# Optimization experiments

Measured on AMD Instinct MI355X. Metric: run time of the kernel, lower is better.

Reference implementation:

```python
import jax, jax.numpy as jnp
import numpy as np

DECAY = 0.8
COMMITMENT_WEIGHT = 1.0
EPS = 1e-5


def setup_inputs() -> dict:
    key = jax.random.key(0)
    k1, k2, k3 = jax.random.split(key, 3)
    B, T, D, K = 16, 2048, 512, 8192
    x = jax.random.normal(k1, (B, T, D), dtype=jnp.float32)
    embed = jax.random.normal(k2, (D, K), dtype=jnp.float32)
    cluster_size = jnp.ones((K,), dtype=jnp.float32)
    embed_avg = jax.random.normal(k3, (D, K), dtype=jnp.float32)
    return {"x": x, "embed": embed, "cluster_size": cluster_size, "embed_avg": embed_avg}


def reference(x, embed, cluster_size, embed_avg):
    B, T, D = x.shape
    K = embed.shape[1]
    flat = x.reshape(-1, D)  # [N, D]

    # squared L2 distance to each code: ||f||^2 - 2 f.e + ||e||^2  -> [N, K]
    dist = (flat * flat).sum(-1, keepdims=True) \
        - 2.0 * (flat @ embed) \
        + (embed * embed).sum(0, keepdims=True)
    embed_ind = jnp.argmin(dist, axis=1)  # [N] (== argmax of -dist)

    quantize = jnp.take(embed.T, embed_ind, axis=0).reshape(B, T, D)

    # ---- EMA codebook statistics (training-mode buffer updates) ----
    onehot_sum = jnp.zeros((K,), dtype=flat.dtype).at[embed_ind].add(1.0)  # [K]
    # flat.T @ onehot == segment-sum of tokens per code, transposed -> [D, K]
    embed_sum = jax.ops.segment_sum(flat, embed_ind, num_segments=K).T
    new_cluster_size = cluster_size * DECAY + (1.0 - DECAY) * onehot_sum
    new_embed_avg = embed_avg * DECAY + (1.0 - DECAY) * embed_sum
    n = new_cluster_size.sum()
    cs = (new_cluster_size + EPS) / (n + K * EPS) * n
    new_embed = new_embed_avg / cs[None, :]
    # (random re-init of unused codes is omitted: non-deterministic side effect)

    commitment_loss = jnp.mean((jax.lax.stop_gradient(quantize) - x) ** 2) * COMMITMENT_WEIGHT
    quantize_st = x + jax.lax.stop_gradient(quantize - x)  # straight-through

    return (quantize_st, embed_ind.reshape(B, T), commitment_loss,
            new_embed, new_cluster_size, new_embed_avg)
```

## Files before the change

### kernel.cpp

```cpp
#include <hip/hip_runtime.h>

#define NTOK   32768
#define DDIM   512
#define KCODES 8192
#define DK     (DDIM * KCODES)
#define DECAYF 0.8f
#define EPSF   1e-5f

using short8 = __attribute__((ext_vector_type(8))) short;
using f32x4  = __attribute__((ext_vector_type(4))) float;

#define WS_ESUMT   0
#define WS_ONEHOT  DK
#define WS_ENORM   (DK + 8192)
#define WS_SCAL    (DK + 16384)
#define WS_PART    (DK + 16400)
#define WS_EMBEDT  (WS_PART + 2 * NTOK)
#define WS_EHI     (WS_EMBEDT + DK)
#define WS_ELO     (WS_EHI + DK / 2)
#define WS_ZERO_BYTES ((size_t)(DK + 16400) * 4)

__device__ __forceinline__ unsigned short bf16rne(float f) {
  unsigned u = __float_as_uint(f);
  unsigned r = u + 0x7FFFu + ((u >> 16) & 1u);
  return (unsigned short)(r >> 16);
}

__device__ __forceinline__ void gload_lds16(const unsigned short* g, unsigned short* l) {
  __builtin_amdgcn_global_load_lds(
      (const __attribute__((address_space(1))) unsigned int*)g,
      (__attribute__((address_space(3))) unsigned int*)l, 16, 0, 0);
}

__global__ __launch_bounds__(256) void split_x_kernel(
    const float* __restrict__ x, unsigned short* __restrict__ hi,
    unsigned short* __restrict__ lo) {
  const size_t i = ((size_t)blockIdx.x * 256 + threadIdx.x) * 8;
  const float4 v0 = *(const float4*)&x[i];
  const float4 v1 = *(const float4*)&x[i + 4];
  const float v[8] = {v0.x, v0.y, v0.z, v0.w, v1.x, v1.y, v1.z, v1.w};
  unsigned short h[8], l[8];
#pragma unroll
  for (int j = 0; j < 8; ++j) {
    h[j] = bf16rne(v[j]);
    l[j] = bf16rne(v[j] - __uint_as_float((unsigned)h[j] << 16));
  }
  uint4 H, L;
  H.x = h[0] | ((unsigned)h[1] << 16); H.y = h[2] | ((unsigned)h[3] << 16);
  H.z = h[4] | ((unsigned)h[5] << 16); H.w = h[6] | ((unsigned)h[7] << 16);
  L.x = l[0] | ((unsigned)l[1] << 16); L.y = l[2] | ((unsigned)l[3] << 16);
  L.z = l[4] | ((unsigned)l[5] << 16); L.w = l[6] | ((unsigned)l[7] << 16);
  *(uint4*)&hi[i] = H;
  *(uint4*)&lo[i] = L;
}

__global__ __launch_bounds__(256) void transpose_split_kernel(
    const float* __restrict__ embed, float* __restrict__ embedT,
    unsigned short* __restrict__ ehi, unsigned short* __restrict__ elo,
    float* __restrict__ e_norm) {
  __shared__ float tile[32][33];
  __shared__ float part[8][32];
  const int k0 = blockIdx.x * 32;
  const int d0 = blockIdx.y * 32;
  const int tx = threadIdx.x;
  const int ty = threadIdx.y;
  float sq = 0.f;
#pragma unroll
  for (int j = 0; j < 4; ++j) {
    const int dl = ty + j * 8;
    const float v = embed[(size_t)(d0 + dl) * KCODES + k0 + tx];
    tile[dl][tx] = v;
    sq += v * v;
  }
  part[ty][tx] = sq;
  __syncthreads();
  if (ty == 0) {
    float s = 0.f;
#pragma unroll
    for (int j = 0; j < 8; ++j) s += part[j][tx];
    atomicAdd(&e_norm[k0 + tx], s);
  }
#pragma unroll
  for (int j = 0; j < 4; ++j) {
    const int kl = ty + j * 8;
    const size_t idx = (size_t)(k0 + kl) * DDIM + d0 + tx;
    const float v = tile[tx][kl];
    embedT[idx] = v;
    const unsigned short h = bf16rne(v);
    ehi[idx] = h;
    elo[idx] = bf16rne(v - __uint_as_float((unsigned)h << 16));
  }
}

__global__ __launch_bounds__(256) void argmin_mfma_kernel(
    const unsigned short* __restrict__ xhi, const unsigned short* __restrict__ xlo,
    const unsigned short* __restrict__ ehi, const unsigned short* __restrict__ elo,
    const float* __restrict__ e_norm, unsigned long long* __restrict__ partials) {
  __shared__ unsigned short Ahs[128 * 32];
  __shared__ unsigned short Als[128 * 32];
  __shared__ unsigned short Bhs[128 * 32];
  __shared__ unsigned short Bls[128 * 32];

  const int t    = threadIdx.x;
  const int wid  = t >> 6;
  const int lid  = t & 63;
  const int kblk = blockIdx.x;
  const int tokbase = blockIdx.y * 128;
  const int kbase   = kblk * 128;

  const int wrow = wid >> 1, wcol = wid & 1;
  const int m16  = lid & 15, kq = lid >> 4;

  const int srow = lid >> 2;
  const int gcol = ((lid & 3) ^ ((srow >> 1) & 3)) * 8;

  const int fsw = (kq ^ ((m16 >> 1) & 3)) * 8;

  f32x4 acc[4][4];
#pragma unroll
  for (int i = 0; i < 4; ++i)
#pragma unroll
    for (int j = 0; j < 4; ++j) acc[i][j] = (f32x4)0.f;

  const unsigned short* Ahg = xhi + (size_t)tokbase * DDIM;
  const unsigned short* Alg = xlo + (size_t)tokbase * DDIM;
  const unsigned short* Bhg = ehi + (size_t)kbase * DDIM;
  const unsigned short* Blg = elo + (size_t)kbase * DDIM;

#pragma unroll 1
  for (int d0 = 0; d0 < DDIM; d0 += 32) {
    __syncthreads();
#pragma unroll
    for (int p = 0; p < 2; ++p) {
      const int chunk = wid + p * 4;
      const size_t go = (size_t)(chunk * 16 + srow) * DDIM + d0 + gcol;
      gload_lds16(Ahg + go, &Ahs[chunk * 512]);
      gload_lds16(Alg + go, &Als[chunk * 512]);
      gload_lds16(Bhg + go, &Bhs[chunk * 512]);
      gload_lds16(Blg + go, &Bls[chunk * 512]);
    }
    __syncthreads();
    short8 bh[4], bl[4];
#pragma unroll
    for (int j = 0; j < 4; ++j) {
      const int r = (wcol * 64 + j * 16 + m16) * 32 + fsw;
      bh[j] = *(const short8*)&Bhs[r];
      bl[j] = *(const short8*)&Bls[r];
    }
#pragma unroll
    for (int i = 0; i < 4; ++i) {
      const int r = (wrow * 64 + i * 16 + m16) * 32 + fsw;
      const short8 ah = *(const short8*)&Ahs[r];
      const short8 al = *(const short8*)&Als[r];
#pragma unroll
      for (int j = 0; j < 4; ++j) {
        acc[i][j] = __builtin_amdgcn_mfma_f32_16x16x32_bf16(ah, bh[j], acc[i][j], 0, 0, 0);
        acc[i][j] = __builtin_amdgcn_mfma_f32_16x16x32_bf16(ah, bl[j], acc[i][j], 0, 0, 0);
        acc[i][j] = __builtin_amdgcn_mfma_f32_16x16x32_bf16(al, bh[j], acc[i][j], 0, 0, 0);
      }
    }
  }

  float en[4];
#pragma unroll
  for (int j = 0; j < 4; ++j)
    en[j] = e_norm[kbase + wcol * 64 + j * 16 + m16];

  __syncthreads();
  unsigned long long* red = (unsigned long long*)Ahs;
#pragma unroll
  for (int i = 0; i < 4; ++i) {
#pragma unroll
    for (int r = 0; r < 4; ++r) {
      unsigned long long best = 0xFFFFFFFFFFFFFFFFull;
#pragma unroll
      for (int j = 0; j < 4; ++j) {
        const float s = en[j] - 2.0f * acc[i][j][r];
        unsigned u = __float_as_uint(s);
        u = (u & 0x80000000u) ? ~u : (u | 0x80000000u);
        const unsigned k = (unsigned)(kbase + wcol * 64 + j * 16 + m16);
        const unsigned long long c = ((unsigned long long)u << 32) | k;
        best = (c < best) ? c : best;
      }
#pragma unroll
      for (int s = 1; s < 16; s <<= 1) {
        const unsigned long long c = __shfl_xor(best, s);
        best = (c < best) ? c : best;
      }
      if (m16 == 0)
        red[(wrow * 64 + i * 16 + kq * 4 + r) * 2 + wcol] = best;
    }
  }
  __syncthreads();
  if (t < 128) {
    const unsigned long long a0 = red[t * 2], a1 = red[t * 2 + 1];
    const unsigned long long m = (a0 < a1) ? a0 : a1;
    atomicMin(&partials[tokbase + t], m);
  }
}

__global__ __launch_bounds__(128) void gather_stats_kernel(
    const float* __restrict__ x, const float* __restrict__ embedT,
    const unsigned long long* __restrict__ partials,
    float* __restrict__ quant_out, float* __restrict__ indf_out,
    float* __restrict__ embed_sumT, float* __restrict__ onehot,
    float* __restrict__ scal) {
  const int n = blockIdx.x;
  __shared__ int s_ind;
  __shared__ float wsum[2];
  if (threadIdx.x == 0) {
    const int k = (int)(partials[n] & 0xFFFFFFFFull);
    s_ind = k;
    indf_out[n] = (float)k;
    atomicAdd(&onehot[k], 1.0f);
  }
  __syncthreads();
  const int k = s_ind;
  const int d4 = threadIdx.x * 4;
  const float4 e  = *(const float4*)&embedT[(size_t)k * DDIM + d4];
  const float4 xv = *(const float4*)&x[(size_t)n * DDIM + d4];
  *(float4*)&quant_out[(size_t)n * DDIM + d4] = e;
  atomicAdd(&embed_sumT[(size_t)k * DDIM + d4 + 0], xv.x);
  atomicAdd(&embed_sumT[(size_t)k * DDIM + d4 + 1], xv.y);
  atomicAdd(&embed_sumT[(size_t)k * DDIM + d4 + 2], xv.z);
  atomicAdd(&embed_sumT[(size_t)k * DDIM + d4 + 3], xv.w);
  const float dx0 = e.x - xv.x, dx1 = e.y - xv.y, dx2 = e.z - xv.z, dx3 = e.w - xv.w;
  float ls = dx0 * dx0 + dx1 * dx1 + dx2 * dx2 + dx3 * dx3;
#pragma unroll
  for (int off = 32; off > 0; off >>= 1) ls += __shfl_down(ls, off);
  if ((threadIdx.x & 63) == 0) wsum[threadIdx.x >> 6] = ls;
  __syncthreads();
  if (threadIdx.x == 0) atomicAdd(&scal[0], wsum[0] + wsum[1]);
}

__global__ __launch_bounds__(256) void cluster_kernel(
    const float* __restrict__ cluster_size, const float* __restrict__ onehot,
    float* __restrict__ ncs_out, float* __restrict__ scal) {
  const int k = blockIdx.x * 256 + threadIdx.x;
  const float v = cluster_size[k] * DECAYF + (1.0f - DECAYF) * onehot[k];
  ncs_out[k] = v;
  float s = v;
#pragma unroll
  for (int off = 32; off > 0; off >>= 1) s += __shfl_down(s, off);
  __shared__ float w[4];
  if ((threadIdx.x & 63) == 0) w[threadIdx.x >> 6] = s;
  __syncthreads();
  if (threadIdx.x == 0) atomicAdd(&scal[1], w[0] + w[1] + w[2] + w[3]);
}

__global__ __launch_bounds__(256) void finalize_kernel(
    const float* __restrict__ embed_avg, const float* __restrict__ embed_sumT,
    const float* __restrict__ ncs, const float* __restrict__ scal,
    float* __restrict__ out_embed, float* __restrict__ out_avg,
    float* __restrict__ out_loss) {
  const int idx = blockIdx.x * 256 + threadIdx.x;
  const int d = idx >> 13;
  const int k = idx & (KCODES - 1);
  const float ea = embed_avg[idx];
  const float es = embed_sumT[(size_t)k * DDIM + d];
  const float nea = DECAYF * ea + (1.0f - DECAYF) * es;
  out_avg[idx] = nea;
  const float nsum = scal[1];
  const float cs = (ncs[k] + EPSF) / (nsum + (float)KCODES * EPSF) * nsum;
  out_embed[idx] = nea / cs;
  if (idx == 0) out_loss[0] = scal[0] * (1.0f / ((float)NTOK * (float)DDIM));
}

extern "C" void kernel_launch(void* const* d_in, const int* in_sizes, int n_in,
                              void* d_out, int out_size, void* d_ws, size_t ws_size,
                              hipStream_t stream) {
  (void)in_sizes; (void)n_in; (void)out_size; (void)ws_size;
  const float* x            = (const float*)d_in[0];
  const float* embed        = (const float*)d_in[1];
  const float* cluster_size = (const float*)d_in[2];
  const float* embed_avg    = (const float*)d_in[3];

  float* out = (float*)d_out;
  float* out_quant = out;
  float* out_indf  = out + 16777216;
  float* out_loss  = out + 16777216 + 32768;
  float* out_embed = out + 16777216 + 32768 + 1;
  float* out_ncs   = out_embed + DK;
  float* out_avg   = out_ncs + KCODES;

  float* ws = (float*)d_ws;
  float* esumT  = ws + WS_ESUMT;
  float* onehot = ws + WS_ONEHOT;
  float* e_norm = ws + WS_ENORM;
  float* scal   = ws + WS_SCAL;
  unsigned long long* partials = (unsigned long long*)(ws + WS_PART);
  float* embedT = ws + WS_EMBEDT;
  unsigned short* ehi = (unsigned short*)(ws + WS_EHI);
  unsigned short* elo = (unsigned short*)(ws + WS_ELO);

  unsigned short* xhi = (unsigned short*)d_out;
  unsigned short* xlo = xhi + (size_t)NTOK * DDIM;

  hipMemsetAsync(d_ws, 0, WS_ZERO_BYTES, stream);
  hipMemsetAsync((char*)d_ws + (size_t)WS_PART * 4, 0xFF, (size_t)NTOK * 8, stream);

  split_x_kernel<<<NTOK * DDIM / 8 / 256, 256, 0, stream>>>(x, xhi, xlo);
  transpose_split_kernel<<<dim3(KCODES / 32, DDIM / 32), dim3(32, 8), 0, stream>>>(
      embed, embedT, ehi, elo, e_norm);

  argmin_mfma_kernel<<<dim3(64, 256), 256, 0, stream>>>(
      xhi, xlo, ehi, elo, e_norm, partials);

  gather_stats_kernel<<<NTOK, 128, 0, stream>>>(
      x, embedT, partials, out_quant, out_indf, esumT, onehot, scal);

  cluster_kernel<<<KCODES / 256, 256, 0, stream>>>(cluster_size, onehot, out_ncs, scal);

  finalize_kernel<<<DK / 256, 256, 0, stream>>>(
      embed_avg, esumT, out_ncs, scal, out_embed, out_avg, out_loss);
}
```

Measured before the change: 1.569 ms.

## Triple-buffer argmin GEMM with 128x256 tiles and interleaved prefetch phases

Rewrites the split-bf16 argmin MFMA kernel to use 512-thread blocks covering 128 tokens by 256 codes. Global-to-LDS loads go into a three-stage ring buffer and are issued in slices between four MFMA phases, with explicit vmcnt waits, barriers and setprio. The aim is to hide global load latency behind matrix math and to raise reuse of each token tile across more codes. The cost is more LDS per block (about 144KB), which limits residency, plus hand-tuned wait counts that must match the number of loads in flight.

```diff
diff --git a/kernel.cpp b/kernel.cpp
--- a/kernel.cpp
+++ b/kernel.cpp
@@ -92,28 +92,29 @@
   }
 }
 
-__global__ __launch_bounds__(256) void argmin_mfma_kernel(
+#define MFMA(d, a, b) d = __builtin_amdgcn_mfma_f32_16x16x32_bf16(a, b, d, 0, 0, 0)
+
+__global__ __launch_bounds__(512, 2) void argmin_mfma_kernel(
     const unsigned short* __restrict__ xhi, const unsigned short* __restrict__ xlo,
     const unsigned short* __restrict__ ehi, const unsigned short* __restrict__ elo,
     const float* __restrict__ e_norm, unsigned long long* __restrict__ partials) {
-  __shared__ unsigned short Ahs[128 * 32];
-  __shared__ unsigned short Als[128 * 32];
-  __shared__ unsigned short Bhs[128 * 32];
-  __shared__ unsigned short Bls[128 * 32];
-
-  const int t    = threadIdx.x;
-  const int wid  = t >> 6;
-  const int lid  = t & 63;
-  const int kblk = blockIdx.x;
+  __shared__ unsigned short Ah[3][128 * 32];
+  __shared__ unsigned short Al[3][128 * 32];
+  __shared__ unsigned short Bh[3][256 * 32];
+  __shared__ unsigned short Bl[3][256 * 32];
+
+  const int tid = threadIdx.x;
+  const int wid = tid >> 6;
+  const int lid = tid & 63;
+  const int kbase   = blockIdx.x * 256;
   const int tokbase = blockIdx.y * 128;
-  const int kbase   = kblk * 128;
-
-  const int wrow = wid >> 1, wcol = wid & 1;
-  const int m16  = lid & 15, kq = lid >> 4;
+
+  const int wrow = wid >> 2;
+  const int wcol = wid & 3;
+  const int m16 = lid & 15, kq = lid >> 4;
 
   const int srow = lid >> 2;
   const int gcol = ((lid & 3) ^ ((srow >> 1) & 3)) * 8;
-
   const int fsw = (kq ^ ((m16 >> 1) & 3)) * 8;
 
   f32x4 acc[4][4];
@@ -122,43 +123,107 @@
 #pragma unroll
     for (int j = 0; j < 4; ++j) acc[i][j] = (f32x4)0.f;
 
-  const unsigned short* Ahg = xhi + (size_t)tokbase * DDIM;
-  const unsigned short* Alg = xlo + (size_t)tokbase * DDIM;
-  const unsigned short* Bhg = ehi + (size_t)kbase * DDIM;
-  const unsigned short* Blg = elo + (size_t)kbase * DDIM;
+  const unsigned short* Ahg  = xhi + (size_t)(tokbase + wid * 16 + srow) * DDIM + gcol;
+  const unsigned short* Alg  = xlo + (size_t)(tokbase + wid * 16 + srow) * DDIM + gcol;
+  const unsigned short* Bhg0 = ehi + (size_t)(kbase + wid * 16 + srow) * DDIM + gcol;
+  const unsigned short* Bhg1 = ehi + (size_t)(kbase + (wid + 8) * 16 + srow) * DDIM + gcol;
+  const unsigned short* Blg0 = elo + (size_t)(kbase + wid * 16 + srow) * DDIM + gcol;
+  const unsigned short* Blg1 = elo + (size_t)(kbase + (wid + 8) * 16 + srow) * DDIM + gcol;
+
+  const int aoff = (wrow * 64 + m16) * 32 + fsw;
+  const int boff = (wcol * 64 + m16) * 32 + fsw;
+
+  gload_lds16(Ahg,       &Ah[0][wid << 9]);
+  gload_lds16(Alg,       &Al[0][wid << 9]);
+  gload_lds16(Bhg0,      &Bh[0][wid << 9]);
+  gload_lds16(Bhg1,      &Bh[0][(wid + 8) << 9]);
+  gload_lds16(Blg0,      &Bl[0][wid << 9]);
+  gload_lds16(Blg1,      &Bl[0][(wid + 8) << 9]);
+  gload_lds16(Ahg  + 32, &Ah[1][wid << 9]);
+  gload_lds16(Alg  + 32, &Al[1][wid << 9]);
+  gload_lds16(Bhg0 + 32, &Bh[1][wid << 9]);
+  gload_lds16(Bhg1 + 32, &Bh[1][(wid + 8) << 9]);
+  gload_lds16(Blg0 + 32, &Bl[1][wid << 9]);
+  gload_lds16(Blg1 + 32, &Bl[1][(wid + 8) << 9]);
 
 #pragma unroll 1
-  for (int d0 = 0; d0 < DDIM; d0 += 32) {
-    __syncthreads();
-#pragma unroll
-    for (int p = 0; p < 2; ++p) {
-      const int chunk = wid + p * 4;
-      const size_t go = (size_t)(chunk * 16 + srow) * DDIM + d0 + gcol;
-      gload_lds16(Ahg + go, &Ahs[chunk * 512]);
-      gload_lds16(Alg + go, &Als[chunk * 512]);
-      gload_lds16(Bhg + go, &Bhs[chunk * 512]);
-      gload_lds16(Blg + go, &Bls[chunk * 512]);
+  for (int t = 0; t < 16; ++t) {
+    const int cur = t % 3;
+    const int pf  = (t + 2) % 3;
+    const int pfo = (t + 2) * 32;
+    const bool dopf = (t + 2) < 16;
+
+    if (t < 15) { asm volatile("s_waitcnt vmcnt(6)" ::: "memory"); }
+    else        { asm volatile("s_waitcnt vmcnt(0)" ::: "memory"); }
+    __builtin_amdgcn_s_barrier();
+
+    const short8 a0h = *(const short8*)&Ah[cur][aoff];
+    const short8 a1h = *(const short8*)&Ah[cur][aoff + 512];
+    const short8 a0l = *(const short8*)&Al[cur][aoff];
+    const short8 a1l = *(const short8*)&Al[cur][aoff + 512];
+    const short8 b0h = *(const short8*)&Bh[cur][boff];
+    const short8 b1h = *(const short8*)&Bh[cur][boff + 512];
+    const short8 b0l = *(const short8*)&Bl[cur][boff];
+    const short8 b1l = *(const short8*)&Bl[cur][boff + 512];
+    if (dopf) {
+      gload_lds16(Ahg + pfo, &Ah[pf][wid << 9]);
+      gload_lds16(Alg + pfo, &Al[pf][wid << 9]);
     }
-    __syncthreads();
-    short8 bh[4], bl[4];
-#pragma unroll
-    for (int j = 0; j < 4; ++j) {
-      const int r = (wcol * 64 + j * 16 + m16) * 32 + fsw;
-      bh[j] = *(const short8*)&Bhs[r];
-      bl[j] = *(const short8*)&Bls[r];
+    __builtin_amdgcn_s_barrier();
+    asm volatile("s_waitcnt lgkmcnt(0)" ::: "memory");
+    __builtin_amdgcn_sched_barrier(0);
+    __builtin_amdgcn_s_setprio(1);
+    MFMA(acc[0][0], a0h, b0h); MFMA(acc[0][0], a0h, b0l); MFMA(acc[0][0], a0l, b0h);
+    MFMA(acc[0][1], a0h, b1h); MFMA(acc[0][1], a0h, b1l); MFMA(acc[0][1], a0l, b1h);
+    MFMA(acc[1][0], a1h, b0h); MFMA(acc[1][0], a1h, b0l); MFMA(acc[1][0], a1l, b0h);
+    MFMA(acc[1][1], a1h, b1h); MFMA(acc[1][1], a1h, b1l); MFMA(acc[1][1], a1l, b1h);
+    __builtin_amdgcn_s_setprio(0);
+    __builtin_amdgcn_s_barrier();
+
+    const short8 b2h = *(const short8*)&Bh[cur][boff + 1024];
+    const short8 b3h = *(const short8*)&Bh[cur][boff + 1536];
+    const short8 b2l = *(const short8*)&Bl[cur][boff + 1024];
+    const short8 b3l = *(const short8*)&Bl[cur][boff + 1536];
+    if (dopf) {
+      gload_lds16(Bhg0 + pfo, &Bh[pf][wid << 9]);
+      gload_lds16(Bhg1 + pfo, &Bh[pf][(wid + 8) << 9]);
     }
-#pragma unroll
-    for (int i = 0; i < 4; ++i) {
-      const int r = (wrow * 64 + i * 16 + m16) * 32 + fsw;
-      const short8 ah = *(const short8*)&Ahs[r];
-      const short8 al = *(const short8*)&Als[r];
-#pragma unroll
-      for (int j = 0; j < 4; ++j) {
-        acc[i][j] = __builtin_amdgcn_mfma_f32_16x16x32_bf16(ah, bh[j], acc[i][j], 0, 0, 0);
-        acc[i][j] = __builtin_amdgcn_mfma_f32_16x16x32_bf16(ah, bl[j], acc[i][j], 0, 0, 0);
-        acc[i][j] = __builtin_amdgcn_mfma_f32_16x16x32_bf16(al, bh[j], acc[i][j], 0, 0, 0);
-      }
-    }
+    __builtin_amdgcn_s_barrier();
+    asm volatile("s_waitcnt lgkmcnt(0)" ::: "memory");
+    __builtin_amdgcn_sched_barrier(0);
+    __builtin_amdgcn_s_setprio(1);
+    MFMA(acc[0][2], a0h, b2h); MFMA(acc[0][2], a0h, b2l); MFMA(acc[0][2], a0l, b2h);
+    MFMA(acc[0][3], a0h, b3h); MFMA(acc[0][3], a0h, b3l); MFMA(acc[0][3], a0l, b3h);
+    MFMA(acc[1][2], a1h, b2h); MFMA(acc[1][2], a1h, b2l); MFMA(acc[1][2], a1l, b2h);
+    MFMA(acc[1][3], a1h, b3h); MFMA(acc[1][3], a1h, b3l); MFMA(acc[1][3], a1l, b3h);
+    __builtin_amdgcn_s_setprio(0);
+    __builtin_amdgcn_s_barrier();
+
+    const short8 c0h = *(const short8*)&Ah[cur][aoff + 1024];
+    const short8 c1h = *(const short8*)&Ah[cur][aoff + 1536];
+    const short8 c0l = *(const short8*)&Al[cur][aoff + 1024];
+    const short8 c1l = *(const short8*)&Al[cur][aoff + 1536];
+    if (dopf) gload_lds16(Blg0 + pfo, &Bl[pf][wid << 9]);
+    __builtin_amdgcn_s_barrier();
+    asm volatile("s_waitcnt lgkmcnt(0)" ::: "memory");
+    __builtin_amdgcn_sched_barrier(0);
+    __builtin_amdgcn_s_setprio(1);
+    MFMA(acc[2][2], c0h, b2h); MFMA(acc[2][2], c0h, b2l); MFMA(acc[2][2], c0l, b2h);
+    MFMA(acc[2][3], c0h, b3h); MFMA(acc[2][3], c0h, b3l); MFMA(acc[2][3], c0l, b3h);
+    MFMA(acc[3][2], c1h, b2h); MFMA(acc[3][2], c1h, b2l); MFMA(acc[3][2], c1l, b2h);
+    MFMA(acc[3][3], c1h, b3h); MFMA(acc[3][3], c1h, b3l); MFMA(acc[3][3], c1l, b3h);
+    __builtin_amdgcn_s_setprio(0);
+    __builtin_amdgcn_s_barrier();
+
+    if (dopf) gload_lds16(Blg1 + pfo, &Bl[pf][(wid + 8) << 9]);
+    __builtin_amdgcn_s_barrier();
+    __builtin_amdgcn_s_setprio(1);
+    MFMA(acc[2][0], c0h, b0h); MFMA(acc[2][0], c0h, b0l); MFMA(acc[2][0], c0l, b0h);
+    MFMA(acc[2][1], c0h, b1h); MFMA(acc[2][1], c0h, b1l); MFMA(acc[2][1], c0l, b1h);
+    MFMA(acc[3][0], c1h, b0h); MFMA(acc[3][0], c1h, b0l); MFMA(acc[3][0], c1l, b0h);
+    MFMA(acc[3][1], c1h, b1h); MFMA(acc[3][1], c1h, b1l); MFMA(acc[3][1], c1l, b1h);
+    __builtin_amdgcn_s_setprio(0);
+    __builtin_amdgcn_s_barrier();
   }
 
   float en[4];
@@ -167,7 +232,7 @@
     en[j] = e_norm[kbase + wcol * 64 + j * 16 + m16];
 
   __syncthreads();
-  unsigned long long* red = (unsigned long long*)Ahs;
+  unsigned long long* red = (unsigned long long*)&Ah[0][0];
 #pragma unroll
   for (int i = 0; i < 4; ++i) {
 #pragma unroll
@@ -188,14 +253,18 @@
         best = (c < best) ? c : best;
       }
       if (m16 == 0)
-        red[(wrow * 64 + i * 16 + kq * 4 + r) * 2 + wcol] = best;
+        red[(wrow * 64 + i * 16 + kq * 4 + r) * 4 + wcol] = best;
     }
   }
   __syncthreads();
-  if (t < 128) {
-    const unsigned long long a0 = red[t * 2], a1 = red[t * 2 + 1];
-    const unsigned long long m = (a0 < a1) ? a0 : a1;
-    atomicMin(&partials[tokbase + t], m);
+  if (tid < 128) {
+    unsigned long long m = red[tid * 4];
+#pragma unroll
+    for (int c = 1; c < 4; ++c) {
+      const unsigned long long v = red[tid * 4 + c];
+      m = (v < m) ? v : m;
+    }
+    atomicMin(&partials[tokbase + tid], m);
   }
 }
 
@@ -303,7 +372,7 @@
   transpose_split_kernel<<<dim3(KCODES / 32, DDIM / 32), dim3(32, 8), 0, stream>>>(
       embed, embedT, ehi, elo, e_norm);
 
-  argmin_mfma_kernel<<<dim3(64, 256), 256, 0, stream>>>(
+  argmin_mfma_kernel<<<dim3(KCODES / 256, NTOK / 128), 512, 0, stream>>>(
       xhi, xlo, ehi, elo, e_norm, partials);
 
   gather_stats_kernel<<<NTOK, 128, 0, stream>>>(
```

Measured after the change: 1.623 ms. 3.5% more time.

## Replace atomic segment-sum with counting-sort token lists and tiled finalize transpose

Applied to the files above, without the earlier changes.

Instead of scattering every token's 512 floats into the per-code sum with float atomics, the code now builds per-code token lists: it scans the counts into offsets, scatters token ids with an integer atomic cursor, and then one block per code sums its tokens' rows without atomics. This also removes the 16 MB memset of the embed_sum buffer, since every row is now written directly. The finalize kernel reads embed_sumT through a shared-memory transposed tile, so its loads are coalesced. In exchange it adds three small launches, a serial single-block scan, and per-code load imbalance when counts are skewed.

```diff
diff --git a/kernel.cpp b/kernel.cpp
--- a/kernel.cpp
+++ b/kernel.cpp
@@ -18,7 +18,6 @@
 #define WS_EMBEDT  (WS_PART + 2 * NTOK)
 #define WS_EHI     (WS_EMBEDT + DK)
 #define WS_ELO     (WS_EHI + DK / 2)
-#define WS_ZERO_BYTES ((size_t)(DK + 16400) * 4)
 
 __device__ __forceinline__ unsigned short bf16rne(float f) {
   unsigned u = __float_as_uint(f);
@@ -199,12 +198,11 @@
   }
 }
 
-__global__ __launch_bounds__(128) void gather_stats_kernel(
+__global__ __launch_bounds__(128) void gather_quant_kernel(
     const float* __restrict__ x, const float* __restrict__ embedT,
     const unsigned long long* __restrict__ partials,
     float* __restrict__ quant_out, float* __restrict__ indf_out,
-    float* __restrict__ embed_sumT, float* __restrict__ onehot,
-    float* __restrict__ scal) {
+    float* __restrict__ onehot, float* __restrict__ scal) {
   const int n = blockIdx.x;
   __shared__ int s_ind;
   __shared__ float wsum[2];
@@ -220,10 +218,6 @@
   const float4 e  = *(const float4*)&embedT[(size_t)k * DDIM + d4];
   const float4 xv = *(const float4*)&x[(size_t)n * DDIM + d4];
   *(float4*)&quant_out[(size_t)n * DDIM + d4] = e;
-  atomicAdd(&embed_sumT[(size_t)k * DDIM + d4 + 0], xv.x);
-  atomicAdd(&embed_sumT[(size_t)k * DDIM + d4 + 1], xv.y);
-  atomicAdd(&embed_sumT[(size_t)k * DDIM + d4 + 2], xv.z);
-  atomicAdd(&embed_sumT[(size_t)k * DDIM + d4 + 3], xv.w);
   const float dx0 = e.x - xv.x, dx1 = e.y - xv.y, dx2 = e.z - xv.z, dx3 = e.w - xv.w;
   float ls = dx0 * dx0 + dx1 * dx1 + dx2 * dx2 + dx3 * dx3;
 #pragma unroll
@@ -231,6 +225,61 @@
   if ((threadIdx.x & 63) == 0) wsum[threadIdx.x >> 6] = ls;
   __syncthreads();
   if (threadIdx.x == 0) atomicAdd(&scal[0], wsum[0] + wsum[1]);
+}
+
+__global__ __launch_bounds__(256) void scan_kernel(
+    const float* __restrict__ counts, unsigned* __restrict__ offsets,
+    unsigned* __restrict__ cursor) {
+  __shared__ unsigned part[256];
+  __shared__ unsigned base[256];
+  const int t = threadIdx.x;
+  unsigned c[32];
+  unsigned s = 0;
+#pragma unroll
+  for (int j = 0; j < 32; ++j) {
+    c[j] = (unsigned)counts[t * 32 + j];
+    s += c[j];
+  }
+  part[t] = s;
+  __syncthreads();
+  if (t == 0) {
+    unsigned r = 0;
+    for (int i = 0; i < 256; ++i) { base[i] = r; r += part[i]; }
+  }
+  __syncthreads();
+  unsigned r = base[t];
+#pragma unroll
+  for (int j = 0; j < 32; ++j) {
+    offsets[t * 32 + j] = r;
+    cursor[t * 32 + j]  = r;
+    r += c[j];
+  }
+}
+
+__global__ __launch_bounds__(256) void scatter_kernel(
+    const unsigned long long* __restrict__ partials,
+    unsigned* __restrict__ cursor, unsigned* __restrict__ toklist) {
+  const int n = blockIdx.x * 256 + threadIdx.x;
+  const int k = (int)(partials[n] & 0xFFFFFFFFull);
+  const unsigned pos = atomicAdd(&cursor[k], 1u);
+  toklist[pos] = n;
+}
+
+__global__ __launch_bounds__(128) void segsum_kernel(
+    const float* __restrict__ x, const float* __restrict__ counts,
+    const unsigned* __restrict__ offsets, const unsigned* __restrict__ toklist,
+    float* __restrict__ esumT) {
+  const int c = blockIdx.x;
+  const unsigned cnt = (unsigned)counts[c];
+  const unsigned beg = offsets[c];
+  const int d4 = threadIdx.x * 4;
+  float4 acc = {0.f, 0.f, 0.f, 0.f};
+  for (unsigned t = 0; t < cnt; ++t) {
+    const unsigned n = toklist[beg + t];
+    const float4 v = *(const float4*)&x[(size_t)n * DDIM + d4];
+    acc.x += v.x; acc.y += v.y; acc.z += v.z; acc.w += v.w;
+  }
+  *(float4*)&esumT[(size_t)c * DDIM + d4] = acc;
 }
 
 __global__ __launch_bounds__(256) void cluster_kernel(
@@ -253,17 +302,29 @@
     const float* __restrict__ ncs, const float* __restrict__ scal,
     float* __restrict__ out_embed, float* __restrict__ out_avg,
     float* __restrict__ out_loss) {
-  const int idx = blockIdx.x * 256 + threadIdx.x;
-  const int d = idx >> 13;
-  const int k = idx & (KCODES - 1);
-  const float ea = embed_avg[idx];
-  const float es = embed_sumT[(size_t)k * DDIM + d];
-  const float nea = DECAYF * ea + (1.0f - DECAYF) * es;
-  out_avg[idx] = nea;
+  __shared__ float tile[32][33];
+  const int k0 = blockIdx.x * 32;
+  const int d0 = blockIdx.y * 32;
+  const int tx = threadIdx.x;
+  const int ty = threadIdx.y;
+#pragma unroll
+  for (int j = 0; j < 4; ++j) {
+    const int kl = ty + j * 8;
+    tile[kl][tx] = embed_sumT[(size_t)(k0 + kl) * DDIM + d0 + tx];
+  }
   const float nsum = scal[1];
-  const float cs = (ncs[k] + EPSF) / (nsum + (float)KCODES * EPSF) * nsum;
-  out_embed[idx] = nea / cs;
-  if (idx == 0) out_loss[0] = scal[0] * (1.0f / ((float)NTOK * (float)DDIM));
+  const float csv = (ncs[k0 + tx] + EPSF) / (nsum + (float)KCODES * EPSF) * nsum;
+  __syncthreads();
+#pragma unroll
+  for (int j = 0; j < 4; ++j) {
+    const int dl = ty + j * 8;
+    const size_t idx = (size_t)(d0 + dl) * KCODES + k0 + tx;
+    const float nea = DECAYF * embed_avg[idx] + (1.0f - DECAYF) * tile[tx][dl];
+    out_avg[idx] = nea;
+    out_embed[idx] = nea / csv;
+  }
+  if (blockIdx.x == 0 && blockIdx.y == 0 && tx == 0 && ty == 0)
+    out_loss[0] = scal[0] * (1.0f / ((float)NTOK * (float)DDIM));
 }
 
 extern "C" void kernel_launch(void* const* d_in, const int* in_sizes, int n_in,
@@ -293,10 +354,14 @@
   unsigned short* ehi = (unsigned short*)(ws + WS_EHI);
   unsigned short* elo = (unsigned short*)(ws + WS_ELO);
 
+  unsigned* offsets = (unsigned*)(ws + WS_EHI);
+  unsigned* cursor  = offsets + KCODES;
+  unsigned* toklist = cursor + KCODES;
+
   unsigned short* xhi = (unsigned short*)d_out;
   unsigned short* xlo = xhi + (size_t)NTOK * DDIM;
 
-  hipMemsetAsync(d_ws, 0, WS_ZERO_BYTES, stream);
+  hipMemsetAsync((char*)d_ws + (size_t)DK * 4, 0, (size_t)16400 * 4, stream);
   hipMemsetAsync((char*)d_ws + (size_t)WS_PART * 4, 0xFF, (size_t)NTOK * 8, stream);
 
   split_x_kernel<<<NTOK * DDIM / 8 / 256, 256, 0, stream>>>(x, xhi, xlo);
@@ -306,11 +371,15 @@
   argmin_mfma_kernel<<<dim3(64, 256), 256, 0, stream>>>(
       xhi, xlo, ehi, elo, e_norm, partials);
 
-  gather_stats_kernel<<<NTOK, 128, 0, stream>>>(
-      x, embedT, partials, out_quant, out_indf, esumT, onehot, scal);
+  gather_quant_kernel<<<NTOK, 128, 0, stream>>>(
+      x, embedT, partials, out_quant, out_indf, onehot, scal);
+
+  scan_kernel<<<1, 256, 0, stream>>>(onehot, offsets, cursor);
+  scatter_kernel<<<NTOK / 256, 256, 0, stream>>>(partials, cursor, toklist);
+  segsum_kernel<<<KCODES, 128, 0, stream>>>(x, onehot, offsets, toklist, esumT);
 
   cluster_kernel<<<KCODES / 256, 256, 0, stream>>>(cluster_size, onehot, out_ncs, scal);
 
-  finalize_kernel<<<DK / 256, 256, 0, stream>>>(
+  finalize_kernel<<<dim3(KCODES / 32, DDIM / 32), dim3(32, 8), 0, stream>>>(
       embed_avg, esumT, out_ncs, scal, out_embed, out_avg, out_loss);
 }
```

After: 1.779 ms. 13.4% more time.

## Fuse prep stages, drop memsets and embedT, tile finalize transpose

Applied to the files above, without the earlier changes.

Merges the x split, the embed transpose/split, the workspace zeroing and the cluster-size partial sums into one prep kernel, which removes the two memsets and several launches. Embed norms are written as per-slice partials and summed inside the argmin kernel instead of using atomics. The fp32 embedT copy is dropped, and the gather reconstructs the codes from the bf16 hi+lo pair; this is not bit-exact with fp32. Finalize now uses a shared-memory tile transpose so its reads of embed_sumT are coalesced, and it folds in the cluster-size computation, with the total computed from the known token count.

```diff
diff --git a/kernel.cpp b/kernel.cpp
--- a/kernel.cpp
+++ b/kernel.cpp
@@ -10,15 +10,13 @@
 using short8 = __attribute__((ext_vector_type(8))) short;
 using f32x4  = __attribute__((ext_vector_type(4))) float;
 
-#define WS_ESUMT   0
-#define WS_ONEHOT  DK
-#define WS_ENORM   (DK + 8192)
-#define WS_SCAL    (DK + 16384)
-#define WS_PART    (DK + 16400)
-#define WS_EMBEDT  (WS_PART + 2 * NTOK)
-#define WS_EHI     (WS_EMBEDT + DK)
-#define WS_ELO     (WS_EHI + DK / 2)
-#define WS_ZERO_BYTES ((size_t)(DK + 16400) * 4)
+#define WS_ESUMT  0
+#define WS_ONEHOT DK
+#define WS_ENP    (DK + 8192)
+#define WS_SCAL   (DK + 8192 + 131072)
+#define WS_PART   (WS_SCAL + 64)
+#define WS_EHI    (WS_PART + 2 * NTOK)
+#define WS_ELO    (WS_EHI + DK / 2)
 
 __device__ __forceinline__ unsigned short bf16rne(float f) {
   unsigned u = __float_as_uint(f);
@@ -32,70 +30,98 @@
       (__attribute__((address_space(3))) unsigned int*)l, 16, 0, 0);
 }
 
-__global__ __launch_bounds__(256) void split_x_kernel(
-    const float* __restrict__ x, unsigned short* __restrict__ hi,
-    unsigned short* __restrict__ lo) {
-  const size_t i = ((size_t)blockIdx.x * 256 + threadIdx.x) * 8;
-  const float4 v0 = *(const float4*)&x[i];
-  const float4 v1 = *(const float4*)&x[i + 4];
-  const float v[8] = {v0.x, v0.y, v0.z, v0.w, v1.x, v1.y, v1.z, v1.w};
-  unsigned short h[8], l[8];
-#pragma unroll
-  for (int j = 0; j < 8; ++j) {
-    h[j] = bf16rne(v[j]);
-    l[j] = bf16rne(v[j] - __uint_as_float((unsigned)h[j] << 16));
-  }
-  uint4 H, L;
-  H.x = h[0] | ((unsigned)h[1] << 16); H.y = h[2] | ((unsigned)h[3] << 16);
-  H.z = h[4] | ((unsigned)h[5] << 16); H.w = h[6] | ((unsigned)h[7] << 16);
-  L.x = l[0] | ((unsigned)l[1] << 16); L.y = l[2] | ((unsigned)l[3] << 16);
-  L.z = l[4] | ((unsigned)l[5] << 16); L.w = l[6] | ((unsigned)l[7] << 16);
-  *(uint4*)&hi[i] = H;
-  *(uint4*)&lo[i] = L;
-}
-
-__global__ __launch_bounds__(256) void transpose_split_kernel(
-    const float* __restrict__ embed, float* __restrict__ embedT,
+__global__ __launch_bounds__(256) void prep_kernel(
+    const float* __restrict__ x, const float* __restrict__ embed,
+    const float* __restrict__ cluster_size,
+    unsigned short* __restrict__ xhi, unsigned short* __restrict__ xlo,
     unsigned short* __restrict__ ehi, unsigned short* __restrict__ elo,
-    float* __restrict__ e_norm) {
+    float* __restrict__ enp, float* __restrict__ esumT,
+    float* __restrict__ onehot, float* __restrict__ scal,
+    unsigned long long* __restrict__ partials) {
   __shared__ float tile[32][33];
   __shared__ float part[8][32];
-  const int k0 = blockIdx.x * 32;
-  const int d0 = blockIdx.y * 32;
-  const int tx = threadIdx.x;
-  const int ty = threadIdx.y;
-  float sq = 0.f;
-#pragma unroll
-  for (int j = 0; j < 4; ++j) {
-    const int dl = ty + j * 8;
-    const float v = embed[(size_t)(d0 + dl) * KCODES + k0 + tx];
-    tile[dl][tx] = v;
-    sq += v * v;
-  }
-  part[ty][tx] = sq;
-  __syncthreads();
-  if (ty == 0) {
-    float s = 0.f;
-#pragma unroll
-    for (int j = 0; j < 8; ++j) s += part[j][tx];
-    atomicAdd(&e_norm[k0 + tx], s);
-  }
-#pragma unroll
-  for (int j = 0; j < 4; ++j) {
-    const int kl = ty + j * 8;
-    const size_t idx = (size_t)(k0 + kl) * DDIM + d0 + tx;
-    const float v = tile[tx][kl];
-    embedT[idx] = v;
-    const unsigned short h = bf16rne(v);
-    ehi[idx] = h;
-    elo[idx] = bf16rne(v - __uint_as_float((unsigned)h << 16));
+  __shared__ float w[4];
+  const int bid = blockIdx.x;
+  const int tid = threadIdx.x;
+
+  if (bid < 8192) {
+    const size_t i = ((size_t)bid * 256 + tid) * 8;
+    const float4 v0 = *(const float4*)&x[i];
+    const float4 v1 = *(const float4*)&x[i + 4];
+    const float v[8] = {v0.x, v0.y, v0.z, v0.w, v1.x, v1.y, v1.z, v1.w};
+    unsigned short h[8], l[8];
+#pragma unroll
+    for (int j = 0; j < 8; ++j) {
+      h[j] = bf16rne(v[j]);
+      l[j] = bf16rne(v[j] - __uint_as_float((unsigned)h[j] << 16));
+    }
+    uint4 H, L;
+    H.x = h[0] | ((unsigned)h[1] << 16); H.y = h[2] | ((unsigned)h[3] << 16);
+    H.z = h[4] | ((unsigned)h[5] << 16); H.w = h[6] | ((unsigned)h[7] << 16);
+    L.x = l[0] | ((unsigned)l[1] << 16); L.y = l[2] | ((unsigned)l[3] << 16);
+    L.z = l[4] | ((unsigned)l[5] << 16); L.w = l[6] | ((unsigned)l[7] << 16);
+    *(uint4*)&xhi[i] = H;
+    *(uint4*)&xlo[i] = L;
+  } else if (bid < 8192 + 4096) {
+    const int tb = bid - 8192;
+    const int k0 = (tb & 255) * 32;
+    const int d0 = (tb >> 8) * 32;
+    const int tx = tid & 31;
+    const int ty = tid >> 5;
+    float sq = 0.f;
+#pragma unroll
+    for (int j = 0; j < 4; ++j) {
+      const int dl = ty + j * 8;
+      const float v = embed[(size_t)(d0 + dl) * KCODES + k0 + tx];
+      tile[dl][tx] = v;
+      sq += v * v;
+    }
+    part[ty][tx] = sq;
+    __syncthreads();
+    if (ty == 0) {
+      float s = 0.f;
+#pragma unroll
+      for (int j = 0; j < 8; ++j) s += part[j][tx];
+      enp[(size_t)(d0 >> 5) * KCODES + k0 + tx] = s;
+    }
+#pragma unroll
+    for (int j = 0; j < 4; ++j) {
+      const int kl = ty + j * 8;
+      const size_t idx = (size_t)(k0 + kl) * DDIM + d0 + tx;
+      const float v = tile[tx][kl];
+      const unsigned short h = bf16rne(v);
+      ehi[idx] = h;
+      elo[idx] = bf16rne(v - __uint_as_float((unsigned)h << 16));
+    }
+  } else if (bid < 8192 + 4096 + 2048) {
+    const int zb = bid - (8192 + 4096);
+    const size_t off = (size_t)zb * 2048 + (size_t)tid * 8;
+    const float4 z = {0.f, 0.f, 0.f, 0.f};
+    *(float4*)&esumT[off] = z;
+    *(float4*)&esumT[off + 4] = z;
+  } else {
+    const int b = bid - (8192 + 4096 + 2048);
+    onehot[b * 256 + tid] = 0.f;
+    const size_t pbase = (size_t)b * 1024 + (size_t)tid * 4;
+    const ulonglong2 ff = {~0ull, ~0ull};
+    *(ulonglong2*)&partials[pbase] = ff;
+    *(ulonglong2*)&partials[pbase + 2] = ff;
+    float s = cluster_size[b * 256 + tid];
+#pragma unroll
+    for (int off = 32; off > 0; off >>= 1) s += __shfl_down(s, off);
+    if ((tid & 63) == 0) w[tid >> 6] = s;
+    __syncthreads();
+    if (tid == 0) {
+      scal[2 + b] = w[0] + w[1] + w[2] + w[3];
+      if (b == 0) { scal[0] = 0.f; scal[1] = 0.f; }
+    }
   }
 }
 
 __global__ __launch_bounds__(256) void argmin_mfma_kernel(
     const unsigned short* __restrict__ xhi, const unsigned short* __restrict__ xlo,
     const unsigned short* __restrict__ ehi, const unsigned short* __restrict__ elo,
-    const float* __restrict__ e_norm, unsigned long long* __restrict__ partials) {
+    const float* __restrict__ enp, unsigned long long* __restrict__ partials) {
   __shared__ unsigned short Ahs[128 * 32];
   __shared__ unsigned short Als[128 * 32];
   __shared__ unsigned short Bhs[128 * 32];
@@ -113,7 +139,6 @@
 
   const int srow = lid >> 2;
   const int gcol = ((lid & 3) ^ ((srow >> 1) & 3)) * 8;
-
   const int fsw = (kq ^ ((m16 >> 1) & 3)) * 8;
 
   f32x4 acc[4][4];
@@ -163,8 +188,13 @@
 
   float en[4];
 #pragma unroll
-  for (int j = 0; j < 4; ++j)
-    en[j] = e_norm[kbase + wcol * 64 + j * 16 + m16];
+  for (int j = 0; j < 4; ++j) {
+    const int kk = kbase + wcol * 64 + j * 16 + m16;
+    float s = 0.f;
+#pragma unroll
+    for (int b = 0; b < 16; ++b) s += enp[(size_t)b * KCODES + kk];
+    en[j] = s;
+  }
 
   __syncthreads();
   unsigned long long* red = (unsigned long long*)Ahs;
@@ -199,25 +229,34 @@
   }
 }
 
-__global__ __launch_bounds__(128) void gather_stats_kernel(
-    const float* __restrict__ x, const float* __restrict__ embedT,
+__global__ __launch_bounds__(256) void gather_stats_kernel(
+    const float* __restrict__ x, const unsigned short* __restrict__ ehi,
+    const unsigned short* __restrict__ elo,
     const unsigned long long* __restrict__ partials,
     float* __restrict__ quant_out, float* __restrict__ indf_out,
     float* __restrict__ embed_sumT, float* __restrict__ onehot,
     float* __restrict__ scal) {
-  const int n = blockIdx.x;
-  __shared__ int s_ind;
-  __shared__ float wsum[2];
-  if (threadIdx.x == 0) {
+  const int sub = threadIdx.x >> 7;
+  const int t7  = threadIdx.x & 127;
+  const int n   = blockIdx.x * 2 + sub;
+  __shared__ int s_ind[2];
+  __shared__ float wsum[4];
+  if (t7 == 0) {
     const int k = (int)(partials[n] & 0xFFFFFFFFull);
-    s_ind = k;
+    s_ind[sub] = k;
     indf_out[n] = (float)k;
     atomicAdd(&onehot[k], 1.0f);
   }
   __syncthreads();
-  const int k = s_ind;
-  const int d4 = threadIdx.x * 4;
-  const float4 e  = *(const float4*)&embedT[(size_t)k * DDIM + d4];
+  const int k = s_ind[sub];
+  const int d4 = t7 * 4;
+  const ushort4 h4 = *(const ushort4*)&ehi[(size_t)k * DDIM + d4];
+  const ushort4 l4 = *(const ushort4*)&elo[(size_t)k * DDIM + d4];
+  float4 e;
+  e.x = __uint_as_float((unsigned)h4.x << 16) + __uint_as_float((unsigned)l4.x << 16);
+  e.y = __uint_as_float((unsigned)h4.y << 16) + __uint_as_float((unsigned)l4.y << 16);
+  e.z = __uint_as_float((unsigned)h4.z << 16) + __uint_as_float((unsigned)l4.z << 16);
+  e.w = __uint_as_float((unsigned)h4.w << 16) + __uint_as_float((unsigned)l4.w << 16);
   const float4 xv = *(const float4*)&x[(size_t)n * DDIM + d4];
   *(float4*)&quant_out[(size_t)n * DDIM + d4] = e;
   atomicAdd(&embed_sumT[(size_t)k * DDIM + d4 + 0], xv.x);
@@ -230,40 +269,50 @@
   for (int off = 32; off > 0; off >>= 1) ls += __shfl_down(ls, off);
   if ((threadIdx.x & 63) == 0) wsum[threadIdx.x >> 6] = ls;
   __syncthreads();
-  if (threadIdx.x == 0) atomicAdd(&scal[0], wsum[0] + wsum[1]);
-}
-
-__global__ __launch_bounds__(256) void cluster_kernel(
-    const float* __restrict__ cluster_size, const float* __restrict__ onehot,
-    float* __restrict__ ncs_out, float* __restrict__ scal) {
-  const int k = blockIdx.x * 256 + threadIdx.x;
-  const float v = cluster_size[k] * DECAYF + (1.0f - DECAYF) * onehot[k];
-  ncs_out[k] = v;
-  float s = v;
-#pragma unroll
-  for (int off = 32; off > 0; off >>= 1) s += __shfl_down(s, off);
-  __shared__ float w[4];
-  if ((threadIdx.x & 63) == 0) w[threadIdx.x >> 6] = s;
-  __syncthreads();
-  if (threadIdx.x == 0) atomicAdd(&scal[1], w[0] + w[1] + w[2] + w[3]);
+  if (threadIdx.x == 0)
+    atomicAdd(&scal[0], wsum[0] + wsum[1] + wsum[2] + wsum[3]);
 }
 
 __global__ __launch_bounds__(256) void finalize_kernel(
     const float* __restrict__ embed_avg, const float* __restrict__ embed_sumT,
-    const float* __restrict__ ncs, const float* __restrict__ scal,
+    const float* __restrict__ cluster_size, const float* __restrict__ onehot,
+    const float* __restrict__ scal,
     float* __restrict__ out_embed, float* __restrict__ out_avg,
-    float* __restrict__ out_loss) {
-  const int idx = blockIdx.x * 256 + threadIdx.x;
-  const int d = idx >> 13;
-  const int k = idx & (KCODES - 1);
-  const float ea = embed_avg[idx];
-  const float es = embed_sumT[(size_t)k * DDIM + d];
-  const float nea = DECAYF * ea + (1.0f - DECAYF) * es;
-  out_avg[idx] = nea;
-  const float nsum = scal[1];
-  const float cs = (ncs[k] + EPSF) / (nsum + (float)KCODES * EPSF) * nsum;
-  out_embed[idx] = nea / cs;
-  if (idx == 0) out_loss[0] = scal[0] * (1.0f / ((float)NTOK * (float)DDIM));
+    float* __restrict__ out_ncs, float* __restrict__ out_loss) {
+  __shared__ float tile[32][33];
+  __shared__ float sh_nsum;
+  const int k0 = blockIdx.x * 32;
+  const int d0 = blockIdx.y * 32;
+  const int tx = threadIdx.x & 31;
+  const int ty = threadIdx.x >> 5;
+  if (threadIdx.x == 0) {
+    float s = 0.f;
+#pragma unroll
+    for (int b = 0; b < 32; ++b) s += scal[2 + b];
+    sh_nsum = DECAYF * s + (1.0f - DECAYF) * (float)NTOK;
+  }
+#pragma unroll
+  for (int j = 0; j < 4; ++j) {
+    const int kl = ty + j * 8;
+    tile[kl][tx] = embed_sumT[(size_t)(k0 + kl) * DDIM + d0 + tx];
+  }
+  __syncthreads();
+  const float nsum = sh_nsum;
+  const float ncs = DECAYF * cluster_size[k0 + tx] + (1.0f - DECAYF) * onehot[k0 + tx];
+  const float csv = (ncs + EPSF) / (nsum + (float)KCODES * EPSF) * nsum;
+#pragma unroll
+  for (int j = 0; j < 4; ++j) {
+    const int dl = ty + j * 8;
+    const size_t idx = (size_t)(d0 + dl) * KCODES + k0 + tx;
+    const float nea = DECAYF * embed_avg[idx] + (1.0f - DECAYF) * tile[tx][dl];
+    out_avg[idx] = nea;
+    out_embed[idx] = nea / csv;
+  }
+  if (blockIdx.y == 0 && threadIdx.x < 32)
+    out_ncs[k0 + threadIdx.x] =
+        DECAYF * cluster_size[k0 + threadIdx.x] + (1.0f - DECAYF) * onehot[k0 + threadIdx.x];
+  if (blockIdx.x == 0 && blockIdx.y == 0 && threadIdx.x == 0)
+    out_loss[0] = scal[0] * (1.0f / ((float)NTOK * (float)DDIM));
 }
 
 extern "C" void kernel_launch(void* const* d_in, const int* in_sizes, int n_in,
@@ -286,31 +335,25 @@
   float* ws = (float*)d_ws;
   float* esumT  = ws + WS_ESUMT;
   float* onehot = ws + WS_ONEHOT;
-  float* e_norm = ws + WS_ENORM;
+  float* enp    = ws + WS_ENP;
   float* scal   = ws + WS_SCAL;
   unsigned long long* partials = (unsigned long long*)(ws + WS_PART);
-  float* embedT = ws + WS_EMBEDT;
   unsigned short* ehi = (unsigned short*)(ws + WS_EHI);
   unsigned short* elo = (unsigned short*)(ws + WS_ELO);
 
   unsigned short* xhi = (unsigned short*)d_out;
   unsigned short* xlo = xhi + (size_t)NTOK * DDIM;
 
-  hipMemsetAsync(d_ws, 0, WS_ZERO_BYTES, stream);
-  hipMemsetAsync((char*)d_ws + (size_t)WS_PART * 4, 0xFF, (size_t)NTOK * 8, stream);
-
-  split_x_kernel<<<NTOK * DDIM / 8 / 256, 256, 0, stream>>>(x, xhi, xlo);
-  transpose_split_kernel<<<dim3(KCODES / 32, DDIM / 32), dim3(32, 8), 0, stream>>>(
-      embed, embedT, ehi, elo, e_norm);
+  prep_kernel<<<8192 + 4096 + 2048 + 32, 256, 0, stream>>>(
+      x, embed, cluster_size, xhi, xlo, ehi, elo, enp, esumT, onehot, scal, partials);
 
   argmin_mfma_kernel<<<dim3(64, 256), 256, 0, stream>>>(
-      xhi, xlo, ehi, elo, e_norm, partials);
-
-  gather_stats_kernel<<<NTOK, 128, 0, stream>>>(
-      x, embedT, partials, out_quant, out_indf, esumT, onehot, scal);
-
-  cluster_kernel<<<KCODES / 256, 256, 0, stream>>>(cluster_size, onehot, out_ncs, scal);
-
-  finalize_kernel<<<DK / 256, 256, 0, stream>>>(
-      embed_avg, esumT, out_ncs, scal, out_embed, out_avg, out_loss);
-}
+      xhi, xlo, ehi, elo, enp, partials);
+
+  gather_stats_kernel<<<NTOK / 2, 256, 0, stream>>>(
+      x, ehi, elo, partials, out_quant, out_indf, esumT, onehot, scal);
+
+  finalize_kernel<<<dim3(KCODES / 32, DDIM / 32), 256, 0, stream>>>(
+      embed_avg, esumT, cluster_size, onehot, scal,
+      out_embed, out_avg, out_ncs, out_loss);
+}
```

Result: faster. 1.431 ms (-8.8%).
